# Kernel optimization log

Hardware: AMD Instinct MI355X
Metric: run time of the kernel (lower is better)

Reference implementation:

```python
import jax, jax.numpy as jnp
import numpy as np

N_NETS = 76  # 29 h2o + 13 o3 + 9 co2 + 3 n2o + 9 ch4 + 13 u
N_CH = 29
N_KE = [29, 13, 9, 3, 9, 13]
# which composition column each of the 76 nets is scaled by
GAS_OF_NET = np.repeat(np.arange(6), N_KE)
# which output channel each of the 76 tau terms is added into (hardcoded table in subcall)
CHAN_OF_NET = np.concatenate([
    np.arange(29),                                            # h2o[i] -> channel i
    np.array([0, 1, 2, 17, 18, 19, 20, 21, 22, 25, 26, 27, 28]),  # o3
    np.array([0, 1, 2, 5, 6, 9, 10, 13, 14]),                 # co2
    np.array([0, 1, 2]),                                      # n2o
    np.array([0, 1, 2, 3, 4, 7, 8, 11, 12]),                  # ch4
    np.array([0, 1, 2, 15, 16, 17, 18, 19, 20, 21, 22, 27, 28]),  # u
])


def setup_inputs() -> dict:
    key = jax.random.key(0)
    ks = jax.random.split(key, 16)
    B, D_IN, H = 262144, 2, 4
    t_p = jax.random.normal(ks[0], (B, D_IN), dtype=jnp.float32)
    composition = jax.random.uniform(ks[1], (B, 8), dtype=jnp.float32)
    null_lw = jnp.zeros((B, 1), dtype=jnp.float32)
    null_iw = jnp.zeros((B, 1), dtype=jnp.float32)
    # stacked params of the 76 tiny DenseFFNs (hidden [4,4], elu; out 1, softplus)
    W1 = jax.random.normal(ks[2], (N_NETS, D_IN, H), dtype=jnp.float32) * 0.5
    b1 = jax.random.normal(ks[3], (N_NETS, H), dtype=jnp.float32) * 0.05
    W2 = jax.random.normal(ks[4], (N_NETS, H, H), dtype=jnp.float32) * 0.5
    b2 = jax.random.normal(ks[5], (N_NETS, H), dtype=jnp.float32) * 0.05
    W3 = jax.random.uniform(ks[6], (N_NETS, H, 1), minval=-1.0, maxval=1.0, dtype=jnp.float32)
    b3 = jnp.zeros((N_NETS, 1), dtype=jnp.float32)
    # per-channel lw / iw Dense(1) layers (input dim 1)
    W_lw = jax.random.normal(ks[7], (N_CH,), dtype=jnp.float32) * 0.5
    b_lw = jax.random.uniform(ks[8], (N_CH,), minval=0.0, maxval=1.0, dtype=jnp.float32)
    W_iw = jax.random.normal(ks[9], (N_CH,), dtype=jnp.float32) * 0.5
    b_iw = jax.random.uniform(ks[10], (N_CH,), minval=0.0, maxval=1.0, dtype=jnp.float32)
    return {"t_p": t_p, "composition": composition, "null_lw": null_lw, "null_iw": null_iw,
            "W1": W1, "b1": b1, "W2": W2, "b2": b2, "W3": W3, "b3": b3,
            "W_lw": W_lw, "b_lw": b_lw, "W_iw": W_iw, "b_iw": b_iw}


def reference(t_p, composition, null_lw, null_iw, W1, b1, W2, b2, W3, b3, W_lw, b_lw, W_iw, b_iw):
    # all 76 tiny MLPs batched as one einsum chain: [n_nets, B, h]
    h = jax.nn.elu(jnp.einsum('bi,nio->nbo', t_p, W1) + b1[:, None, :])
    h = jax.nn.elu(jnp.einsum('nbi,nio->nbo', h, W2) + b2[:, None, :])
    ke = jax.nn.softplus(jnp.einsum('nbi,nio->nbo', h, W3) + b3[:, None, :])[..., 0]  # [76, B]
    # scale each net's output by its gas concentration, then scatter-add into 29 channels
    tau = ke * composition[:, GAS_OF_NET].T                                  # [76, B]
    tau_gases = jax.ops.segment_sum(tau, jnp.asarray(CHAN_OF_NET), num_segments=N_CH)  # [29, B]
    tau_gases = jnp.transpose(tau_gases)[:, :, None]                          # [B, 29, 1]
    # lw / iw: softplus(null * w_c + b_c) * composition[:, 6 or 7]
    tau_lw = (jax.nn.softplus(null_lw * W_lw[None, :] + b_lw[None, :]) * composition[:, 6:7])[:, :, None]
    tau_iw = (jax.nn.softplus(null_iw * W_iw[None, :] + b_iw[None, :]) * composition[:, 7:8])[:, :, None]
    return (tau_gases, tau_lw, tau_iw)
```

## Files before the change

kernel.cpp:

```cpp
#include <hip/hip_runtime.h>
#include <cstdint>

#define BLOCK 256
#define ROWS 64
#define NRECP 76

typedef float v2f __attribute__((ext_vector_type(2)));
typedef float v4f __attribute__((ext_vector_type(4)));

__device__ __forceinline__ float exp2s(float x) { return __builtin_amdgcn_exp2f(x); }
__device__ __forceinline__ float log2s(float x) { return __builtin_amdgcn_logf(x); }
__device__ __forceinline__ v2f exp22(v2f x) { return (v2f){exp2s(x.x), exp2s(x.y)}; }
__device__ __forceinline__ v2f fma2(v2f a, v2f b, v2f c) { return __builtin_elementwise_fma(a, b, c); }
__device__ __forceinline__ v2f max2(v2f a, v2f b) { return __builtin_elementwise_max(a, b); }
__device__ __forceinline__ v2f min2(v2f a, v2f b) { return __builtin_elementwise_min(a, b); }
__device__ __forceinline__ v2f abs2(v2f a) { return __builtin_elementwise_abs(a); }
__device__ __forceinline__ v2f splat(float s) { return (v2f){s, s}; }

#define LN2 0.6931471805599453f
#define L2E 1.4426950408889634f

constexpr int GAS_[76] = {
    0,0,0,0,0,0,0,0,0,0,0,0,0,0,0,0,0,0,0,0,0,0,0,0,0,0,0,0,0,
    1,1,1,1,1,1,1,1,1,1,1,1,1,
    2,2,2,2,2,2,2,2,2,
    3,3,3,
    4,4,4,4,4,4,4,4,4,
    5,5,5,5,5,5,5,5,5,5,5,5,5};
constexpr int CHAN_[76] = {
    0,1,2,3,4,5,6,7,8,9,10,11,12,13,14,15,16,17,18,19,20,21,22,23,24,25,26,27,28,
    0,1,2,17,18,19,20,21,22,25,26,27,28,
    0,1,2,5,6,9,10,13,14,
    0,1,2,
    0,1,2,3,4,7,8,11,12,
    0,1,2,15,16,17,18,19,20,21,22,27,28};

__global__ void __launch_bounds__(128)
prep_kernel(const float* __restrict__ W1, const float* __restrict__ b1,
            const float* __restrict__ W2, const float* __restrict__ b2,
            const float* __restrict__ W3, const float* __restrict__ b3,
            const float* __restrict__ W_lw, const float* __restrict__ b_lw,
            const float* __restrict__ W_iw, const float* __restrict__ b_iw,
            float* __restrict__ rec)
{
    const int p = threadIdx.x;
    if (p < 38) {
        const int nA = 2 * p, nB = 2 * p + 1;
        float* r = rec + p * NRECP;
        #pragma unroll
        for (int k = 0; k < 8; ++k) {
            r[2 * k]     = W1[nA * 8 + k] * L2E;
            r[2 * k + 1] = W1[nB * 8 + k] * L2E;
        }
        #pragma unroll
        for (int o = 0; o < 4; ++o) {
            r[16 + 2 * o]     = b1[nA * 4 + o] * L2E;
            r[16 + 2 * o + 1] = b1[nB * 4 + o] * L2E;
        }
        #pragma unroll
        for (int k = 0; k < 16; ++k) {
            r[24 + 2 * k]     = W2[nA * 16 + k] * L2E;
            r[24 + 2 * k + 1] = W2[nB * 16 + k] * L2E;
        }
        #pragma unroll
        for (int o = 0; o < 4; ++o) {
            float sA = 0.0f, sB = 0.0f;
            #pragma unroll
            for (int i = 0; i < 4; ++i) {
                sA += W2[nA * 16 + i * 4 + o];
                sB += W2[nB * 16 + i * 4 + o];
            }
            r[56 + 2 * o]     = (b2[nA * 4 + o] - sA) * L2E;
            r[56 + 2 * o + 1] = (b2[nB * 4 + o] - sB) * L2E;
        }
        float s3A = 0.0f, s3B = 0.0f;
        #pragma unroll
        for (int i = 0; i < 4; ++i) {
            r[64 + 2 * i]     = W3[nA * 4 + i] * L2E;  s3A += W3[nA * 4 + i];
            r[64 + 2 * i + 1] = W3[nB * 4 + i] * L2E;  s3B += W3[nB * 4 + i];
        }
        r[72] = (b3[nA] - s3A) * L2E;
        r[73] = (b3[nB] - s3B) * L2E;
        r[74] = 0.0f; r[75] = 0.0f;
    } else if (p < 38 + 29) {
        const int ch = p - 38;
        float* t = rec + 38 * NRECP + ch * 4;
        t[0] = W_lw[ch] * L2E;
        t[1] = b_lw[ch] * L2E;
        t[2] = W_iw[ch] * L2E;
        t[3] = b_iw[ch] * L2E;
    }
}

__device__ __forceinline__ v2f elu_h2(v2f as) {
    return max2(fma2(as, splat(LN2), splat(1.0f)), exp22(min2(as, splat(0.0f))));
}

template<int PS, int PE>
__device__ __forceinline__ void run_pairs(
    const float* __restrict__ rec, float tpx, float tpy,
    const float* cgl2 , float* tau)
{
    const v2f tpx2 = splat(tpx);
    const v2f tpy2 = splat(tpy);
    #pragma unroll
    for (int p = PS; p < PE; ++p) {
        const v2f* __restrict__ RP = (const v2f*)(rec + p * NRECP);
        v2f H1[4];
        #pragma unroll
        for (int o = 0; o < 4; ++o)
            H1[o] = elu_h2(fma2(tpx2, RP[o], fma2(tpy2, RP[4 + o], RP[8 + o])));
        v2f H2[4];
        #pragma unroll
        for (int o = 0; o < 4; ++o) {
            v2f a = RP[28 + o];
            #pragma unroll
            for (int i = 0; i < 4; ++i)
                a = fma2(H1[i], RP[12 + i * 4 + o], a);
            H2[o] = elu_h2(a);
        }
        v2f a3 = RP[36];
        #pragma unroll
        for (int i = 0; i < 4; ++i)
            a3 = fma2(H2[i], RP[32 + i], a3);
        const v2f e = exp22(-abs2(a3));
        const v2f sp = max2(a3, splat(0.0f)) +
                       (v2f){log2s(1.0f + e.x), log2s(1.0f + e.y)};
        tau[CHAN_[2 * p]]     = fmaf(sp.x, cgl2[GAS_[2 * p]],     tau[CHAN_[2 * p]]);
        tau[CHAN_[2 * p + 1]] = fmaf(sp.y, cgl2[GAS_[2 * p + 1]], tau[CHAN_[2 * p + 1]]);
    }
}

template<bool EXACT>
__global__ void __launch_bounds__(BLOCK)
od_kernel(const float* __restrict__ t_p,
          const float* __restrict__ comp,
          const float* __restrict__ null_lw,
          const float* __restrict__ null_iw,
          const float* __restrict__ rec,
          float* __restrict__ out, int B)
{
    __shared__ float stage[2][ROWS * 29];

    const int tid  = threadIdx.x;
    const int wave = tid >> 6;
    const int lane = tid & 63;
    const int base = blockIdx.x * ROWS;
    const int row  = EXACT ? (base + lane)
                           : ((base + lane < B) ? (base + lane) : (B - 1));

    const float2 tp = *reinterpret_cast<const float2*>(t_p + (size_t)row * 2);
    const float4 ca = *reinterpret_cast<const float4*>(comp + (size_t)row * 8);
    const float2 cb = *reinterpret_cast<const float2*>(comp + (size_t)row * 8 + 4);
    const float cgl2[6] = {ca.x * LN2, ca.y * LN2, ca.z * LN2,
                           ca.w * LN2, cb.x * LN2, cb.y * LN2};

    float tau[29];
    #pragma unroll
    for (int i = 0; i < 29; ++i) tau[i] = 0.0f;

    switch (wave) {
        case 0: run_pairs< 0, 10>(rec, tp.x, tp.y, cgl2, tau); break;
        case 1: run_pairs<10, 20>(rec, tp.x, tp.y, cgl2, tau); break;
        case 2: run_pairs<20, 29>(rec, tp.x, tp.y, cgl2, tau); break;
        default: run_pairs<29, 38>(rec, tp.x, tp.y, cgl2, tau); break;
    }

    if (wave < 2) {
        #pragma unroll
        for (int i = 0; i < 29; ++i) stage[wave][lane * 29 + i] = tau[i];
    }
    __syncthreads();
    if (wave >= 2) {
        float* p = stage[wave - 2];
        #pragma unroll
        for (int i = 0; i < 29; ++i) p[lane * 29 + i] += tau[i];
    }
    __syncthreads();

    const size_t obase = (size_t)base * 29;
    const size_t BN = (size_t)B * 29;
    const float* __restrict__ recL = rec + 38 * NRECP;

    if (EXACT) {
        const int t4 = tid * 4;
        #pragma unroll
        for (int it = 0; it < 2; ++it) {
            const int idx = t4 + it * (BLOCK * 4);
            if (idx < ROWS * 29) {
                const v4f s0 = *reinterpret_cast<const v4f*>(&stage[0][idx]);
                const v4f s1 = *reinterpret_cast<const v4f*>(&stage[1][idx]);
                const v4f v0 = s0 + s1;

                float o1[4], o2[4];
                int rr = idx / 29;
                int cc = idx - rr * 29;
                #pragma unroll
                for (int j = 0; j < 4; ++j) {
                    const int grow = base + rr;
                    const float nl = null_lw[grow];
                    const float ni = null_iw[grow];
                    const float c6 = comp[(size_t)grow * 8 + 6] * LN2;
                    const float c7 = comp[(size_t)grow * 8 + 7] * LN2;
                    const v4f L = *reinterpret_cast<const v4f*>(recL + cc * 4);
                    const float alw = fmaf(nl, L.x, L.y);
                    const float aiw = fmaf(ni, L.z, L.w);
                    o1[j] = (fmaxf(alw, 0.0f) + log2s(1.0f + exp2s(-fabsf(alw)))) * c6;
                    o2[j] = (fmaxf(aiw, 0.0f) + log2s(1.0f + exp2s(-fabsf(aiw)))) * c7;
                    if (++cc == 29) { cc = 0; ++rr; }
                }
                const v4f v1 = {o1[0], o1[1], o1[2], o1[3]};
                const v4f v2 = {o2[0], o2[1], o2[2], o2[3]};
                __builtin_nontemporal_store(v0, reinterpret_cast<v4f*>(out + obase + idx));
                __builtin_nontemporal_store(v1, reinterpret_cast<v4f*>(out + BN + obase + idx));
                __builtin_nontemporal_store(v2, reinterpret_cast<v4f*>(out + 2 * BN + obase + idx));
            }
        }
    } else {
        const int rrem0 = B - base;
        const int rrem = rrem0 < 0 ? 0 : (rrem0 > ROWS ? ROWS : rrem0);
        const int lim = rrem * 29;
        for (int idx = tid; idx < lim; idx += BLOCK) {
            out[obase + idx] = stage[0][idx] + stage[1][idx];
            const int r  = idx / 29;
            const int ch = idx - r * 29;
            const int grow = base + r;
            const float nl = null_lw[grow];
            const float ni = null_iw[grow];
            const float c6 = comp[(size_t)grow * 8 + 6] * LN2;
            const float c7 = comp[(size_t)grow * 8 + 7] * LN2;
            const v4f L = *reinterpret_cast<const v4f*>(recL + ch * 4);
            const float alw = fmaf(nl, L.x, L.y);
            const float aiw = fmaf(ni, L.z, L.w);
            out[BN + obase + idx] =
                (fmaxf(alw, 0.0f) + log2s(1.0f + exp2s(-fabsf(alw)))) * c6;
            out[2 * BN + obase + idx] =
                (fmaxf(aiw, 0.0f) + log2s(1.0f + exp2s(-fabsf(aiw)))) * c7;
        }
    }
}

extern "C" void kernel_launch(void* const* d_in, const int* in_sizes, int n_in,
                              void* d_out, int out_size, void* d_ws, size_t ws_size,
                              hipStream_t stream) {
    const float* t_p     = (const float*)d_in[0];
    const float* comp    = (const float*)d_in[1];
    const float* null_lw = (const float*)d_in[2];
    const float* null_iw = (const float*)d_in[3];
    const float* W1      = (const float*)d_in[4];
    const float* b1      = (const float*)d_in[5];
    const float* W2      = (const float*)d_in[6];
    const float* b2      = (const float*)d_in[7];
    const float* W3      = (const float*)d_in[8];
    const float* b3      = (const float*)d_in[9];
    const float* W_lw    = (const float*)d_in[10];
    const float* b_lw    = (const float*)d_in[11];
    const float* W_iw    = (const float*)d_in[12];
    const float* b_iw    = (const float*)d_in[13];
    float* out = (float*)d_out;
    float* rec = (float*)d_ws;

    const int B = in_sizes[0] / 2;

    prep_kernel<<<1, 128, 0, stream>>>(W1, b1, W2, b2, W3, b3,
                                       W_lw, b_lw, W_iw, b_iw, rec);

    const int blocks = (B + ROWS - 1) / ROWS;
    if (B % ROWS == 0)
        od_kernel<true><<<blocks, BLOCK, 0, stream>>>(t_p, comp, null_lw, null_iw,
                                                      rec, out, B);
    else
        od_kernel<false><<<blocks, BLOCK, 0, stream>>>(t_p, comp, null_lw, null_iw,
                                                       rec, out, B);
}
```

Before: 55.28 us.

## Give each wave its own rows and evaluate all nets per thread

Result: slower. 57.84 us (+4.6%).

```diff
diff --git a/kernel.cpp b/kernel.cpp
--- a/kernel.cpp
+++ b/kernel.cpp
@@ -2,7 +2,7 @@
 #include <cstdint>
 
 #define BLOCK 256
-#define ROWS 64
+#define ROWS 256
 #define NRECP 76
 
 typedef float v2f __attribute__((ext_vector_type(2)));
@@ -96,15 +96,14 @@
     return max2(fma2(as, splat(LN2), splat(1.0f)), exp22(min2(as, splat(0.0f))));
 }
 
-template<int PS, int PE>
-__device__ __forceinline__ void run_pairs(
+__device__ __forceinline__ void run_all_pairs(
     const float* __restrict__ rec, float tpx, float tpy,
     const float* cgl2 , float* tau)
 {
     const v2f tpx2 = splat(tpx);
     const v2f tpy2 = splat(tpy);
     #pragma unroll
-    for (int p = PS; p < PE; ++p) {
+    for (int p = 0; p < 38; ++p) {
         const v2f* __restrict__ RP = (const v2f*)(rec + p * NRECP);
         v2f H1[4];
         #pragma unroll
@@ -140,14 +139,14 @@
           const float* __restrict__ rec,
           float* __restrict__ out, int B)
 {
-    __shared__ float stage[2][ROWS * 29];
+    __shared__ float stage[4][64 * 29];
 
     const int tid  = threadIdx.x;
     const int wave = tid >> 6;
     const int lane = tid & 63;
-    const int base = blockIdx.x * ROWS;
-    const int row  = EXACT ? (base + lane)
-                           : ((base + lane < B) ? (base + lane) : (B - 1));
+    const int wbase = blockIdx.x * ROWS + wave * 64;
+    const int row   = EXACT ? (wbase + lane)
+                            : ((wbase + lane < B) ? (wbase + lane) : (B - 1));
 
     const float2 tp = *reinterpret_cast<const float2*>(t_p + (size_t)row * 2);
     const float4 ca = *reinterpret_cast<const float4*>(comp + (size_t)row * 8);
@@ -159,45 +158,29 @@
     #pragma unroll
     for (int i = 0; i < 29; ++i) tau[i] = 0.0f;
 
-    switch (wave) {
-        case 0: run_pairs< 0, 10>(rec, tp.x, tp.y, cgl2, tau); break;
-        case 1: run_pairs<10, 20>(rec, tp.x, tp.y, cgl2, tau); break;
-        case 2: run_pairs<20, 29>(rec, tp.x, tp.y, cgl2, tau); break;
-        default: run_pairs<29, 38>(rec, tp.x, tp.y, cgl2, tau); break;
-    }
-
-    if (wave < 2) {
-        #pragma unroll
-        for (int i = 0; i < 29; ++i) stage[wave][lane * 29 + i] = tau[i];
-    }
-    __syncthreads();
-    if (wave >= 2) {
-        float* p = stage[wave - 2];
-        #pragma unroll
-        for (int i = 0; i < 29; ++i) p[lane * 29 + i] += tau[i];
-    }
-    __syncthreads();
-
-    const size_t obase = (size_t)base * 29;
+    run_all_pairs(rec, tp.x, tp.y, cgl2, tau);
+
+    float* ws = stage[wave];
+    #pragma unroll
+    for (int i = 0; i < 29; ++i) ws[lane * 29 + i] = tau[i];
+
+    const size_t obase = (size_t)wbase * 29;
     const size_t BN = (size_t)B * 29;
     const float* __restrict__ recL = rec + 38 * NRECP;
 
     if (EXACT) {
-        const int t4 = tid * 4;
-        #pragma unroll
-        for (int it = 0; it < 2; ++it) {
-            const int idx = t4 + it * (BLOCK * 4);
-            if (idx < ROWS * 29) {
-                const v4f s0 = *reinterpret_cast<const v4f*>(&stage[0][idx]);
-                const v4f s1 = *reinterpret_cast<const v4f*>(&stage[1][idx]);
-                const v4f v0 = s0 + s1;
+        #pragma unroll
+        for (int it = 0; it < 8; ++it) {
+            const int idx = lane * 4 + it * 256;
+            if (it < 7 || idx < 64 * 29) {
+                const v4f v0 = *reinterpret_cast<const v4f*>(ws + idx);
 
                 float o1[4], o2[4];
                 int rr = idx / 29;
                 int cc = idx - rr * 29;
                 #pragma unroll
                 for (int j = 0; j < 4; ++j) {
-                    const int grow = base + rr;
+                    const int grow = wbase + rr;
                     const float nl = null_lw[grow];
                     const float ni = null_iw[grow];
                     const float c6 = comp[(size_t)grow * 8 + 6] * LN2;
@@ -217,14 +200,14 @@
             }
         }
     } else {
-        const int rrem0 = B - base;
-        const int rrem = rrem0 < 0 ? 0 : (rrem0 > ROWS ? ROWS : rrem0);
+        const int rrem0 = B - wbase;
+        const int rrem = rrem0 < 0 ? 0 : (rrem0 > 64 ? 64 : rrem0);
         const int lim = rrem * 29;
-        for (int idx = tid; idx < lim; idx += BLOCK) {
-            out[obase + idx] = stage[0][idx] + stage[1][idx];
+        for (int idx = lane; idx < lim; idx += 64) {
+            out[obase + idx] = ws[idx];
             const int r  = idx / 29;
             const int ch = idx - r * 29;
-            const int grow = base + r;
+            const int grow = wbase + r;
             const float nl = null_lw[grow];
             const float ni = null_iw[grow];
             const float c6 = comp[(size_t)grow * 8 + 6] * LN2;
```
